# Optimization experiments

Measured on AMD Instinct MI355X. Metric: run time of the kernel, lower is better.

The kernel has to match this reference:

```python
import jax, jax.numpy as jnp
import numpy as np

B, N = 512, 256
NC = N // 2          # number of SOC (friction-cone) constraints
MAX_ITER = 100       # matches module max_iter
POWER_ITERS = 20     # power iterations for Lipschitz constant estimate


def setup_inputs() -> dict:
    key = jax.random.key(0)
    k1, k2, k3, k4 = jax.random.split(key, 4)
    P = jax.random.normal(k1, (B, N, N), dtype=jnp.float32)
    q = jax.random.normal(k2, (B, N, 1), dtype=jnp.float32)
    l_n = jax.random.uniform(k3, (B, NC, 1), dtype=jnp.float32)
    mu = jax.random.uniform(k4, (B, NC, 1), dtype=jnp.float32)
    return {"P": P, "q": q, "l_n": l_n, "mu": mu}


def _solve(P, b, r):
    # minimize 0.5 * ||P l||^2 + b^T l   s.t.  ||l[2i:2i+2]|| <= r[i]
    # via FISTA (accelerated projected gradient); projection onto a product
    # of 2-D balls is closed-form, honoring the block-SOC structure.
    H = jnp.einsum('bki,bkj->bij', P, P)  # [B,N,N] = P^T P (PSD)

    # Lipschitz constant of grad = lambda_max(H) via power iteration
    def power_step(v, _):
        w = jnp.einsum('bij,bj->bi', H, v)
        v = w / (jnp.linalg.norm(w, axis=-1, keepdims=True) + 1e-12)
        return v, None

    v0 = jnp.ones((B, N), dtype=P.dtype)
    v, _ = jax.lax.scan(power_step, v0, None, length=POWER_ITERS)
    Hv = jnp.einsum('bij,bj->bi', H, v)
    L = jnp.sum(v * Hv, axis=-1) / jnp.sum(v * v, axis=-1)  # [B] Rayleigh quotient
    step = 1.0 / (1.05 * jnp.maximum(L, 1e-12))             # [B]

    def project(l):
        pairs = l.reshape(B, NC, 2)
        nrm = jnp.linalg.norm(pairs, axis=-1)               # [B,NC]
        scale = jnp.where(nrm > r, r / jnp.maximum(nrm, 1e-30), 1.0)
        return (pairs * scale[..., None]).reshape(B, N)

    def fista_step(carry, _):
        l, y, t = carry
        g = jnp.einsum('bij,bj->bi', H, y) + b
        l_new = project(y - step[:, None] * g)
        t_new = 0.5 * (1.0 + jnp.sqrt(1.0 + 4.0 * t * t))
        y_new = l_new + ((t - 1.0) / t_new) * (l_new - l)
        return (l_new, y_new, t_new), None

    l0 = project(jnp.zeros_like(b))
    (l, _, _), _ = jax.lax.scan(fista_step, (l0, l0, jnp.float32(1.0)),
                                None, length=MAX_ITER)
    return l  # [B,N]


def reference(P, q, l_n, mu):
    b = q[..., 0]            # [B,N]
    r = (mu * l_n)[..., 0]   # [B,NC] nonneg SOC radii (mu*l_n in the original)
    return _solve(P, b, r)
```

## Files before the change

kernel.cpp:

```cpp
#include <hip/hip_runtime.h>
#include <math.h>


namespace {

constexpr int NDIM = 256;
constexpr int NCON = 128;
constexpr int PITERS = 20;
constexpr int FITERS = 100;

typedef short bf16x8 __attribute__((ext_vector_type(8)));
typedef float f32x4  __attribute__((ext_vector_type(4)));

struct Smem {
    union {
        struct {
            unsigned short fragHi[16 * 64 * 8];
            unsigned short fragLo[16 * 64 * 8];
        };
        float Hbuf[8][32 * 36];
    };
    float red[2][8][256];
    float scal[16];
};

__device__ __forceinline__ unsigned short bf16rne(float x) {
    unsigned u = __float_as_uint(x);
    unsigned r = u + 0x7FFFu + ((u >> 16) & 1u);
    return (unsigned short)(r >> 16);
}

__device__ __forceinline__ float readlane_f(float v, int lane) {
    return __int_as_float(__builtin_amdgcn_readlane(__float_as_int(v), lane));
}

__device__ __forceinline__ void mv_reg(const float (&h)[128], const float (&xs)[32],
                                       float* __restrict__ redw, int l)
{
    float pw0 = 0.f, pw1 = 0.f, pw2 = 0.f, pw3 = 0.f;
#pragma unroll
    for (int j = 0; j < 32; ++j) {
        pw0 = fmaf(h[0 * 32 + j], xs[j], pw0);
        pw1 = fmaf(h[1 * 32 + j], xs[j], pw1);
        pw2 = fmaf(h[2 * 32 + j], xs[j], pw2);
        pw3 = fmaf(h[3 * 32 + j], xs[j], pw3);
    }
    *(float4*)(redw + 4 * l) = make_float4(pw0, pw1, pw2, pw3);
}

__device__ __forceinline__ float2 gather_pair(const float (*red8)[256], int w, int l)
{
    float s0 = 0.f, s1 = 0.f;
#pragma unroll
    for (int c2 = 0; c2 < 8; ++c2) {
        float2 p = *(const float2*)&red8[c2][32 * w + 2 * l];
        s0 += p.x; s1 += p.y;
    }
    return make_float2(s0, s1);
}

__global__ __launch_bounds__(512, 2)
void qcqp_fista(const float* __restrict__ P, const float* __restrict__ q,
                const float* __restrict__ ln_, const float* __restrict__ mu,
                float* __restrict__ out)
{
    __shared__ Smem sm;
    const int b = blockIdx.x;
    const int t = threadIdx.x;
    const int w = t >> 6;
    const int l = t & 63;

    const float* Pb = P + (size_t)b * (NDIM * NDIM);

    const int col  = t & 255;
    const int half = t >> 8;
    const int tile = col >> 4;

    float pf[16];
    auto load_chunk = [&](int cc) {
#pragma unroll
        for (int g = 0; g < 2; ++g) {
            const int qd = 2 * half + g;
            const float* src = Pb + (cc * 32 + qd * 8) * 256 + col;
#pragma unroll
            for (int j = 0; j < 8; ++j) pf[g * 8 + j] = src[j * 256];
        }
    };

    f32x4 acc[16][2];
#pragma unroll
    for (int i = 0; i < 16; ++i)
#pragma unroll
        for (int j = 0; j < 2; ++j)
#pragma unroll
            for (int e = 0; e < 4; ++e) acc[i][j][e] = 0.0f;

    load_chunk(0);
    for (int c = 0; c < 8; ++c) {
#pragma unroll
        for (int g = 0; g < 2; ++g) {
            const int qd = 2 * half + g;
            unsigned hw[4], lw[4];
#pragma unroll
            for (int jp = 0; jp < 4; ++jp) {
                float f0 = pf[g * 8 + 2 * jp], f1 = pf[g * 8 + 2 * jp + 1];
                unsigned short h0 = bf16rne(f0), h1 = bf16rne(f1);
                float r0 = f0 - __uint_as_float((unsigned)h0 << 16);
                float r1 = f1 - __uint_as_float((unsigned)h1 << 16);
                unsigned short lo0 = bf16rne(r0), lo1 = bf16rne(r1);
                hw[jp] = (unsigned)h0 | ((unsigned)h1 << 16);
                lw[jp] = (unsigned)lo0 | ((unsigned)lo1 << 16);
            }
            const int slot = tile * 64 + ((col & 15) + 16 * qd);
            ((uint4*)sm.fragHi)[slot] = make_uint4(hw[0], hw[1], hw[2], hw[3]);
            ((uint4*)sm.fragLo)[slot] = make_uint4(lw[0], lw[1], lw[2], lw[3]);
        }
        __syncthreads();
        if (c < 7) load_chunk(c + 1);

        const bf16x8* FH = (const bf16x8*)sm.fragHi;
        const bf16x8* FL = (const bf16x8*)sm.fragLo;
        bf16x8 bh0 = FH[(2 * w) * 64 + l];
        bf16x8 bl0 = FL[(2 * w) * 64 + l];
        bf16x8 bh1 = FH[(2 * w + 1) * 64 + l];
        bf16x8 bl1 = FL[(2 * w + 1) * 64 + l];
#pragma unroll
        for (int tr = 0; tr < 16; ++tr) {
            bf16x8 ah = FH[tr * 64 + l];
            bf16x8 al = FL[tr * 64 + l];
            acc[tr][0] = __builtin_amdgcn_mfma_f32_16x16x32_bf16(ah, bh0, acc[tr][0], 0, 0, 0);
            acc[tr][0] = __builtin_amdgcn_mfma_f32_16x16x32_bf16(al, bh0, acc[tr][0], 0, 0, 0);
            acc[tr][0] = __builtin_amdgcn_mfma_f32_16x16x32_bf16(ah, bl0, acc[tr][0], 0, 0, 0);
            acc[tr][1] = __builtin_amdgcn_mfma_f32_16x16x32_bf16(ah, bh1, acc[tr][1], 0, 0, 0);
            acc[tr][1] = __builtin_amdgcn_mfma_f32_16x16x32_bf16(al, bh1, acc[tr][1], 0, 0, 0);
            acc[tr][1] = __builtin_amdgcn_mfma_f32_16x16x32_bf16(ah, bl1, acc[tr][1], 0, 0, 0);
        }
        __syncthreads();
    }

    const int qd4 = (l >> 4) * 4;
    const int c16 = l & 15;
    float* Hw = sm.Hbuf[w];
    float h[128];
#pragma unroll
    for (int rc = 0; rc < 8; ++rc) {
#pragma unroll
        for (int tt = 0; tt < 2; ++tt)
#pragma unroll
            for (int tc = 0; tc < 2; ++tc)
#pragma unroll
                for (int reg = 0; reg < 4; ++reg) {
                    int row_local = 16 * tt + qd4 + reg;
                    Hw[row_local * 36 + 16 * tc + c16] = acc[2 * rc + tt][tc][reg];
                }
        if ((l >> 3) == rc) {
            int l2 = l & 7;
#pragma unroll
            for (int e = 0; e < 4; ++e)
#pragma unroll
                for (int jj = 0; jj < 8; ++jj) {
                    float4 v = *(const float4*)&Hw[(4 * l2 + e) * 36 + 4 * jj];
                    h[e * 32 + jj * 4 + 0] = v.x;
                    h[e * 32 + jj * 4 + 1] = v.y;
                    h[e * 32 + jj * 4 + 2] = v.z;
                    h[e * 32 + jj * 4 + 3] = v.w;
                }
        }
    }

    float cy0 = 1.0f, cy1 = 1.0f;
    int phase = 0;
    for (int it = 0; it < PITERS; ++it, ++phase) {
        float xs[32];
#pragma unroll
        for (int j = 0; j < 16; ++j) {
            xs[2 * j]     = readlane_f(cy0, j);
            xs[2 * j + 1] = readlane_f(cy1, j);
        }
        mv_reg(h, xs, sm.red[phase & 1][w], l);
        __syncthreads();
        if (l < 16) {
            float2 s = gather_pair(sm.red[phase & 1], w, l);
            cy0 = s.x * 0.0009765625f;
            cy1 = s.y * 0.0009765625f;
        }
    }

    {
        float xs[32];
#pragma unroll
        for (int j = 0; j < 16; ++j) {
            xs[2 * j]     = readlane_f(cy0, j);
            xs[2 * j + 1] = readlane_f(cy1, j);
        }
        mv_reg(h, xs, sm.red[phase & 1][w], l);
    }
    __syncthreads();
    float n1 = 0.f, n2 = 0.f;
    if (l < 16) {
        float2 hv = gather_pair(sm.red[phase & 1], w, l);
        n1 = cy0 * hv.x + cy1 * hv.y;
        n2 = cy0 * cy0 + cy1 * cy1;
    }
#pragma unroll
    for (int off = 1; off < 64; off <<= 1) {
        n1 += __shfl_xor(n1, off);
        n2 += __shfl_xor(n2, off);
    }
    if (l == 0) { sm.scal[w] = n1; sm.scal[8 + w] = n2; }
    __syncthreads();
    float num = 0.f, den = 0.f;
#pragma unroll
    for (int ww = 0; ww < 8; ++ww) { num += sm.scal[ww]; den += sm.scal[8 + ww]; }
    float L = num / den;
    const float step = 1.0f / (1.05f * fmaxf(L, 1e-12f));
    ++phase;

    float b0 = 0.f, b1 = 0.f, rr = 0.f;
    if (l < 16) {
        float2 q2 = *(const float2*)(q + b * NDIM + 32 * w + 2 * l);
        b0 = q2.x; b1 = q2.y;
        rr = mu[b * NCON + 16 * w + l] * ln_[b * NCON + 16 * w + l];
    }
    float li0 = 0.f, li1 = 0.f, tcur = 1.0f;
    cy0 = 0.0f; cy1 = 0.0f;

    for (int it = 0; it < FITERS; ++it, ++phase) {
        float xs[32];
#pragma unroll
        for (int j = 0; j < 16; ++j) {
            xs[2 * j]     = readlane_f(cy0, j);
            xs[2 * j + 1] = readlane_f(cy1, j);
        }
        mv_reg(h, xs, sm.red[phase & 1][w], l);
        __syncthreads();
        float tn = 0.5f * (1.0f + sqrtf(1.0f + 4.0f * tcur * tcur));
        float ratio = (tcur - 1.0f) / tn;
        tcur = tn;
        if (l < 16) {
            float2 hy = gather_pair(sm.red[phase & 1], w, l);
            float z0 = cy0 - step * (hy.x + b0);
            float z1 = cy1 - step * (hy.y + b1);
            float nrm = sqrtf(z0 * z0 + z1 * z1);
            float scl = (nrm > rr) ? (rr / fmaxf(nrm, 1e-30f)) : 1.0f;
            float l0 = z0 * scl, l1 = z1 * scl;
            float yn0 = l0 + ratio * (l0 - li0);
            float yn1 = l1 + ratio * (l1 - li1);
            li0 = l0; li1 = l1;
            cy0 = yn0; cy1 = yn1;
        }
    }

    if (l < 16)
        *(float2*)(out + b * NDIM + 32 * w + 2 * l) = make_float2(li0, li1);
}

}

extern "C" void kernel_launch(void* const* d_in, const int* in_sizes, int n_in,
                              void* d_out, int out_size, void* d_ws, size_t ws_size,
                              hipStream_t stream) {
    const float* P   = (const float*)d_in[0];
    const float* q   = (const float*)d_in[1];
    const float* l_n = (const float*)d_in[2];
    const float* mu  = (const float*)d_in[3];
    float* out = (float*)d_out;
    qcqp_fista<<<dim3(512), dim3(512), 0, stream>>>(P, q, l_n, mu, out);
}
```

Before: 426.8 us.

## Split H computation into two passes and use packed FMA matvec

The Gram-matrix MFMA phase now runs in two passes of 8 row tiles each, reloading P for the second pass, so only half the accumulators are live at once and register pressure drops. The register-resident H slice is stored interleaved so the matvec can use packed 2-wide FMAs. The projection compares squared norms and uses rsqrt instead of sqrt plus divide. The cost is reading P and redoing the bf16 split twice, plus a slightly different rounding in the projection.

```diff
diff --git a/kernel.cpp b/kernel.cpp
--- a/kernel.cpp
+++ b/kernel.cpp
@@ -11,6 +11,7 @@
 
 typedef short bf16x8 __attribute__((ext_vector_type(8)));
 typedef float f32x4  __attribute__((ext_vector_type(4)));
+typedef float f32x2  __attribute__((ext_vector_type(2)));
 
 struct Smem {
     union {
@@ -34,18 +35,18 @@
     return __int_as_float(__builtin_amdgcn_readlane(__float_as_int(v), lane));
 }
 
-__device__ __forceinline__ void mv_reg(const float (&h)[128], const float (&xs)[32],
-                                       float* __restrict__ redw, int l)
+__device__ __forceinline__ void mv_pk(const float (&h)[128], const float (&xs)[32],
+                                      float* __restrict__ redw, int l)
 {
-    float pw0 = 0.f, pw1 = 0.f, pw2 = 0.f, pw3 = 0.f;
+    const f32x2* h2 = (const f32x2*)h;
+    f32x2 pw01 = {0.f, 0.f}, pw23 = {0.f, 0.f};
 #pragma unroll
     for (int j = 0; j < 32; ++j) {
-        pw0 = fmaf(h[0 * 32 + j], xs[j], pw0);
-        pw1 = fmaf(h[1 * 32 + j], xs[j], pw1);
-        pw2 = fmaf(h[2 * 32 + j], xs[j], pw2);
-        pw3 = fmaf(h[3 * 32 + j], xs[j], pw3);
-    }
-    *(float4*)(redw + 4 * l) = make_float4(pw0, pw1, pw2, pw3);
+        f32x2 xb = {xs[j], xs[j]};
+        pw01 = __builtin_elementwise_fma(h2[2 * j],     xb, pw01);
+        pw23 = __builtin_elementwise_fma(h2[2 * j + 1], xb, pw23);
+    }
+    *(float4*)(redw + 4 * l) = make_float4(pw01.x, pw01.y, pw23.x, pw23.y);
 }
 
 __device__ __forceinline__ float2 gather_pair(const float (*red8)[256], int w, int l)
@@ -87,85 +88,89 @@
         }
     };
 
-    f32x4 acc[16][2];
-#pragma unroll
-    for (int i = 0; i < 16; ++i)
-#pragma unroll
-        for (int j = 0; j < 2; ++j)
-#pragma unroll
-            for (int e = 0; e < 4; ++e) acc[i][j][e] = 0.0f;
-
-    load_chunk(0);
-    for (int c = 0; c < 8; ++c) {
-#pragma unroll
-        for (int g = 0; g < 2; ++g) {
-            const int qd = 2 * half + g;
-            unsigned hw[4], lw[4];
-#pragma unroll
-            for (int jp = 0; jp < 4; ++jp) {
-                float f0 = pf[g * 8 + 2 * jp], f1 = pf[g * 8 + 2 * jp + 1];
-                unsigned short h0 = bf16rne(f0), h1 = bf16rne(f1);
-                float r0 = f0 - __uint_as_float((unsigned)h0 << 16);
-                float r1 = f1 - __uint_as_float((unsigned)h1 << 16);
-                unsigned short lo0 = bf16rne(r0), lo1 = bf16rne(r1);
-                hw[jp] = (unsigned)h0 | ((unsigned)h1 << 16);
-                lw[jp] = (unsigned)lo0 | ((unsigned)lo1 << 16);
-            }
-            const int slot = tile * 64 + ((col & 15) + 16 * qd);
-            ((uint4*)sm.fragHi)[slot] = make_uint4(hw[0], hw[1], hw[2], hw[3]);
-            ((uint4*)sm.fragLo)[slot] = make_uint4(lw[0], lw[1], lw[2], lw[3]);
-        }
-        __syncthreads();
-        if (c < 7) load_chunk(c + 1);
-
-        const bf16x8* FH = (const bf16x8*)sm.fragHi;
-        const bf16x8* FL = (const bf16x8*)sm.fragLo;
-        bf16x8 bh0 = FH[(2 * w) * 64 + l];
-        bf16x8 bl0 = FL[(2 * w) * 64 + l];
-        bf16x8 bh1 = FH[(2 * w + 1) * 64 + l];
-        bf16x8 bl1 = FL[(2 * w + 1) * 64 + l];
-#pragma unroll
-        for (int tr = 0; tr < 16; ++tr) {
-            bf16x8 ah = FH[tr * 64 + l];
-            bf16x8 al = FL[tr * 64 + l];
-            acc[tr][0] = __builtin_amdgcn_mfma_f32_16x16x32_bf16(ah, bh0, acc[tr][0], 0, 0, 0);
-            acc[tr][0] = __builtin_amdgcn_mfma_f32_16x16x32_bf16(al, bh0, acc[tr][0], 0, 0, 0);
-            acc[tr][0] = __builtin_amdgcn_mfma_f32_16x16x32_bf16(ah, bl0, acc[tr][0], 0, 0, 0);
-            acc[tr][1] = __builtin_amdgcn_mfma_f32_16x16x32_bf16(ah, bh1, acc[tr][1], 0, 0, 0);
-            acc[tr][1] = __builtin_amdgcn_mfma_f32_16x16x32_bf16(al, bh1, acc[tr][1], 0, 0, 0);
-            acc[tr][1] = __builtin_amdgcn_mfma_f32_16x16x32_bf16(ah, bl1, acc[tr][1], 0, 0, 0);
-        }
-        __syncthreads();
-    }
-
     const int qd4 = (l >> 4) * 4;
     const int c16 = l & 15;
     float* Hw = sm.Hbuf[w];
     float h[128];
-#pragma unroll
-    for (int rc = 0; rc < 8; ++rc) {
-#pragma unroll
-        for (int tt = 0; tt < 2; ++tt)
-#pragma unroll
-            for (int tc = 0; tc < 2; ++tc)
-#pragma unroll
-                for (int reg = 0; reg < 4; ++reg) {
-                    int row_local = 16 * tt + qd4 + reg;
-                    Hw[row_local * 36 + 16 * tc + c16] = acc[2 * rc + tt][tc][reg];
+
+    load_chunk(0);
+    for (int pass = 0; pass < 2; ++pass) {
+        f32x4 acc[8][2];
+#pragma unroll
+        for (int i = 0; i < 8; ++i)
+#pragma unroll
+            for (int j = 0; j < 2; ++j)
+#pragma unroll
+                for (int e = 0; e < 4; ++e) acc[i][j][e] = 0.0f;
+
+        for (int c = 0; c < 8; ++c) {
+#pragma unroll
+            for (int g = 0; g < 2; ++g) {
+                const int qd = 2 * half + g;
+                unsigned hw[4], lw[4];
+#pragma unroll
+                for (int jp = 0; jp < 4; ++jp) {
+                    float f0 = pf[g * 8 + 2 * jp], f1 = pf[g * 8 + 2 * jp + 1];
+                    unsigned short h0 = bf16rne(f0), h1 = bf16rne(f1);
+                    float r0 = f0 - __uint_as_float((unsigned)h0 << 16);
+                    float r1 = f1 - __uint_as_float((unsigned)h1 << 16);
+                    unsigned short lo0 = bf16rne(r0), lo1 = bf16rne(r1);
+                    hw[jp] = (unsigned)h0 | ((unsigned)h1 << 16);
+                    lw[jp] = (unsigned)lo0 | ((unsigned)lo1 << 16);
                 }
-        if ((l >> 3) == rc) {
-            int l2 = l & 7;
-#pragma unroll
-            for (int e = 0; e < 4; ++e)
-#pragma unroll
-                for (int jj = 0; jj < 8; ++jj) {
-                    float4 v = *(const float4*)&Hw[(4 * l2 + e) * 36 + 4 * jj];
-                    h[e * 32 + jj * 4 + 0] = v.x;
-                    h[e * 32 + jj * 4 + 1] = v.y;
-                    h[e * 32 + jj * 4 + 2] = v.z;
-                    h[e * 32 + jj * 4 + 3] = v.w;
-                }
-        }
+                const int slot = tile * 64 + ((col & 15) + 16 * qd);
+                ((uint4*)sm.fragHi)[slot] = make_uint4(hw[0], hw[1], hw[2], hw[3]);
+                ((uint4*)sm.fragLo)[slot] = make_uint4(lw[0], lw[1], lw[2], lw[3]);
+            }
+            __syncthreads();
+            if (c < 7) load_chunk(c + 1);
+            else if (pass == 0) load_chunk(0);
+
+            const bf16x8* FH = (const bf16x8*)sm.fragHi;
+            const bf16x8* FL = (const bf16x8*)sm.fragLo;
+            bf16x8 bh0 = FH[(2 * w) * 64 + l];
+            bf16x8 bl0 = FL[(2 * w) * 64 + l];
+            bf16x8 bh1 = FH[(2 * w + 1) * 64 + l];
+            bf16x8 bl1 = FL[(2 * w + 1) * 64 + l];
+#pragma unroll
+            for (int tt = 0; tt < 8; ++tt) {
+                bf16x8 ah = FH[(8 * pass + tt) * 64 + l];
+                bf16x8 al = FL[(8 * pass + tt) * 64 + l];
+                acc[tt][0] = __builtin_amdgcn_mfma_f32_16x16x32_bf16(ah, bh0, acc[tt][0], 0, 0, 0);
+                acc[tt][0] = __builtin_amdgcn_mfma_f32_16x16x32_bf16(al, bh0, acc[tt][0], 0, 0, 0);
+                acc[tt][0] = __builtin_amdgcn_mfma_f32_16x16x32_bf16(ah, bl0, acc[tt][0], 0, 0, 0);
+                acc[tt][1] = __builtin_amdgcn_mfma_f32_16x16x32_bf16(ah, bh1, acc[tt][1], 0, 0, 0);
+                acc[tt][1] = __builtin_amdgcn_mfma_f32_16x16x32_bf16(al, bh1, acc[tt][1], 0, 0, 0);
+                acc[tt][1] = __builtin_amdgcn_mfma_f32_16x16x32_bf16(ah, bl1, acc[tt][1], 0, 0, 0);
+            }
+            __syncthreads();
+        }
+
+#pragma unroll
+        for (int rc = 0; rc < 4; ++rc) {
+#pragma unroll
+            for (int s = 0; s < 2; ++s)
+#pragma unroll
+                for (int tc = 0; tc < 2; ++tc)
+#pragma unroll
+                    for (int reg = 0; reg < 4; ++reg)
+                        Hw[(16 * s + qd4 + reg) * 36 + 16 * tc + c16] =
+                            acc[2 * rc + s][tc][reg];
+            if ((l >> 3) == 4 * pass + rc) {
+                int l2 = l & 7;
+#pragma unroll
+                for (int e = 0; e < 4; ++e)
+#pragma unroll
+                    for (int jj = 0; jj < 8; ++jj) {
+                        float4 v = *(const float4*)&Hw[(4 * l2 + e) * 36 + 4 * jj];
+                        h[4 * (4 * jj + 0) + e] = v.x;
+                        h[4 * (4 * jj + 1) + e] = v.y;
+                        h[4 * (4 * jj + 2) + e] = v.z;
+                        h[4 * (4 * jj + 3) + e] = v.w;
+                    }
+            }
+        }
+        if (pass == 0) __syncthreads();
     }
 
     float cy0 = 1.0f, cy1 = 1.0f;
@@ -177,7 +182,7 @@
             xs[2 * j]     = readlane_f(cy0, j);
             xs[2 * j + 1] = readlane_f(cy1, j);
         }
-        mv_reg(h, xs, sm.red[phase & 1][w], l);
+        mv_pk(h, xs, sm.red[phase & 1][w], l);
         __syncthreads();
         if (l < 16) {
             float2 s = gather_pair(sm.red[phase & 1], w, l);
@@ -193,7 +198,7 @@
             xs[2 * j]     = readlane_f(cy0, j);
             xs[2 * j + 1] = readlane_f(cy1, j);
         }
-        mv_reg(h, xs, sm.red[phase & 1][w], l);
+        mv_pk(h, xs, sm.red[phase & 1][w], l);
     }
     __syncthreads();
     float n1 = 0.f, n2 = 0.f;
@@ -222,6 +227,7 @@
         b0 = q2.x; b1 = q2.y;
         rr = mu[b * NCON + 16 * w + l] * ln_[b * NCON + 16 * w + l];
     }
+    const float rr2 = rr * rr;
     float li0 = 0.f, li1 = 0.f, tcur = 1.0f;
     cy0 = 0.0f; cy1 = 0.0f;
 
@@ -232,7 +238,7 @@
             xs[2 * j]     = readlane_f(cy0, j);
             xs[2 * j + 1] = readlane_f(cy1, j);
         }
-        mv_reg(h, xs, sm.red[phase & 1][w], l);
+        mv_pk(h, xs, sm.red[phase & 1][w], l);
         __syncthreads();
         float tn = 0.5f * (1.0f + sqrtf(1.0f + 4.0f * tcur * tcur));
         float ratio = (tcur - 1.0f) / tn;
@@ -241,8 +247,8 @@
             float2 hy = gather_pair(sm.red[phase & 1], w, l);
             float z0 = cy0 - step * (hy.x + b0);
             float z1 = cy1 - step * (hy.y + b1);
-            float nrm = sqrtf(z0 * z0 + z1 * z1);
-            float scl = (nrm > rr) ? (rr / fmaxf(nrm, 1e-30f)) : 1.0f;
+            float n2sq = z0 * z0 + z1 * z1;
+            float scl = (n2sq > rr2) ? (rr * rsqrtf(n2sq)) : 1.0f;
             float l0 = z0 * scl, l1 = z1 * scl;
             float yn0 = l0 + ratio * (l0 - li0);
             float yn1 = l1 + ratio * (l1 - li1);
```

Measured after the change: 640.3 us. 50.0% more time.
